# Performance work log

Hardware: AMD Instinct MI355X
Metric: run time of the kernel (lower is better)

Reference implementation:

```python
import jax, jax.numpy as jnp
import numpy as np

SD = 4            # sqrt of capsule dim (matrix pose)
STRIDE = 2
LN_EPS = 1e-5


def _unfold(x, k, s):
    # x: [B, N, H, W, A] -> patches [B, N, k, k, Ho, Wo, A]  (matches torch unfold+permute)
    B, N, H, W, A = x.shape
    Ho = (H - k) // s + 1
    Wo = (W - k) // s + 1
    ih = np.arange(Ho)[:, None] * s + np.arange(k)   # [Ho, k]
    iw = np.arange(Wo)[:, None] * s + np.arange(k)   # [Wo, k]
    p = x[:, :, ih]               # [B, N, Ho, k, W, A]
    p = p[:, :, :, :, iw]         # [B, N, Ho, k, Wo, k, A]
    return p.transpose(0, 1, 3, 5, 2, 4, 6)


def _layer_norm(v, g, b):
    mu = jnp.mean(v, axis=-1, keepdims=True)
    var = jnp.mean(jnp.square(v - mu), axis=-1, keepdims=True)
    return (v - mu) * jax.lax.rsqrt(var + LN_EPS) * g + b


def setup_inputs() -> dict:
    key = jax.random.key(0)
    k0, k1, k2 = jax.random.split(key, 3)
    B, N, H, W, A = 64, 32, 16, 16, 16     # batch, in caps, spatial, pose dim
    K, M, D = 3, 32, 16                     # kernel, out caps (conv), out pose dim
    Ho = Wo = (H - K) // STRIDE + 1         # 7
    Nfc, Cls = M * Ho * Wo, 10              # 1568 fc input caps, 10 classes
    x = jax.random.normal(k0, (B, N, H, W, A), dtype=jnp.float32)
    c_conv = np.sqrt(M / (SD * N * K * K)).astype(np.float32)
    w_conv = c_conv * jax.random.normal(k1, (K, K, N, SD, SD, M), dtype=jnp.float32)
    c_fc = np.sqrt(Cls / (SD * Nfc)).astype(np.float32)
    w_fc = c_fc * jax.random.normal(k2, (Nfc, SD, SD, Cls), dtype=jnp.float32)
    return {
        "x": x, "w_conv": w_conv, "w_fc": w_fc,
        "ln1_g": jnp.ones((D,), jnp.float32), "ln1_b": jnp.zeros((D,), jnp.float32),
        "ln2_g": jnp.ones((D,), jnp.float32), "ln2_b": jnp.zeros((D,), jnp.float32),
        "num_routing": 3,
    }


def reference(x, w_conv, w_fc, ln1_g, ln1_b, ln2_g, ln2_b, num_routing):
    B = x.shape[0]
    K, _, N, _, _, M = w_conv.shape
    D = SD * SD
    scale = 1.0 / np.sqrt(D)

    # ---------------- CapsuleCONV (matrix pose) ----------------
    patches = _unfold(x, K, STRIDE)                       # [B,N,K,K,Ho,Wo,A]
    Ho, Wo = patches.shape[4], patches.shape[5]
    inp = patches.reshape(B, N, K, K, Ho, Wo, SD, SD)     # bnklhwax

    # pass 0: uniform routing prior (softmax of zeros) == 1/M
    v = jnp.einsum('bnklhwax,klnxdm->bmhwad', inp, w_conv) / M
    v = _layer_norm(v.reshape(B, M, Ho, Wo, D), ln1_g, ln1_b)
    for _ in range(num_routing - 1):
        v4 = v.reshape(B, M, Ho, Wo, SD, SD)
        logits = jnp.einsum('bnklhwax,klnxdm,bmhwad->bnklmhw', inp, w_conv, v4) * scale
        qk = jax.nn.softmax(logits, axis=4)
        qk = qk / (jnp.sum(qk, axis=4, keepdims=True) + 1e-10)
        v = jnp.einsum('bnklmhw,bnklhwax,klnxdm->bmhwad', qk, inp, w_conv)
        v = _layer_norm(v.reshape(B, M, Ho, Wo, D), ln1_g, ln1_b)

    # ---------------- CapsuleFC (matrix pose) ----------------
    # [B,M,Ho,Wo,D] -> permute(0,4,1,2,3) -> flatten -> [B, M*Ho*Wo, D]
    fc_in = v.transpose(0, 4, 1, 2, 3).reshape(B, D, M * Ho * Wo).transpose(0, 2, 1)
    Nfc, Cls = w_fc.shape[0], w_fc.shape[3]
    _in = fc_in.reshape(B, Nfc, SD, SD)                   # bnax

    u = jnp.einsum('bnax,nxdm->bmad', _in, w_fc) / Cls
    u = _layer_norm(u.reshape(B, Cls, D), ln2_g, ln2_b)
    for _ in range(num_routing - 1):
        u4 = u.reshape(B, Cls, SD, SD)
        logits = jnp.einsum('bnax,nxdm,bmad->bnm', _in, w_fc, u4) * scale
        qk = jax.nn.softmax(logits, axis=2)
        qk = qk / (jnp.sum(qk, axis=2, keepdims=True) + 1e-10)
        u = jnp.einsum('bnm,bnax,nxdm->bmad', qk, _in, w_fc)
        u = _layer_norm(u.reshape(B, Cls, D), ln2_g, ln2_b)

    return u  # [B, num_classes, out_d_capsules]
```

## Files before the change

### kernel.cpp

```cpp
#include <hip/hip_runtime.h>
#include <hip/hip_bf16.h>


#define LN_EPS 1e-5f

typedef _Float16 h2 __attribute__((ext_vector_type(2)));

__device__ __forceinline__ unsigned packh2(float a, float b) {
    const unsigned short ua = __builtin_bit_cast(unsigned short, (_Float16)a);
    const unsigned short ub = __builtin_bit_cast(unsigned short, (_Float16)b);
    return (unsigned)ua | ((unsigned)ub << 16);
}

__device__ __forceinline__ float fdot2u(unsigned a, unsigned b, float c) {
    float d;
    asm("v_dot2_f32_f16 %0, %1, %2, %3" : "=v"(d) : "v"(a), "v"(b), "v"(c));
    return d;
}

template <int CTRL>
__device__ __forceinline__ float dpp_add(float x) {
    return x + __builtin_bit_cast(float,
        __builtin_amdgcn_mov_dpp(__builtin_bit_cast(int, x), CTRL, 0xF, 0xF, false));
}
__device__ __forceinline__ float row16_sum(float x) {
    x = dpp_add<0xB1>(x);
    x = dpp_add<0x4E>(x);
    x = dpp_add<0x124>(x);
    x = dpp_add<0x128>(x);
    return x;
}
__device__ __forceinline__ float swz_xor16(float x) {
    return __builtin_bit_cast(float,
        __builtin_amdgcn_ds_swizzle(__builtin_bit_cast(int, x), 0x401F));
}

__global__ __launch_bounds__(256) void transpose_wconv(
    const float* __restrict__ wconv, unsigned short* __restrict__ wTh)
{
    const int i = blockIdx.x * 256 + threadIdx.x;
    if (i < 147456) {
        const int x = i & 3, d = (i >> 2) & 3, mm = (i >> 4) & 31, r = i >> 9;
        const int n = r / 9, kl = r % 9;
        const float v = wconv[((kl * 32 + n) * 16 + x * 4 + d) * 32 + mm];
        wTh[i] = __builtin_bit_cast(unsigned short, (_Float16)v);
    }
}
__global__ __launch_bounds__(256) void transpose_wfc(
    const float* __restrict__ wfc, float* __restrict__ wT2b)
{
    const int j = blockIdx.x * 256 + threadIdx.x;
    if (j < 401408) {
        const int xd = j & 15, mm = (j >> 4) & 15, n = j >> 8;
        const int x = xd >> 2, dd = xd & 3;
        wT2b[j] = (mm < 10) ? wfc[((n * 4 + x) * 4 + dd) * 10 + mm] : 0.f;
    }
}
__global__ __launch_bounds__(256) void transpose_weights(
    const float* __restrict__ wconv, const float* __restrict__ wfc,
    unsigned short* __restrict__ wTh, float* __restrict__ wT2b)
{
    const int blk = blockIdx.x;
    if (blk < 576) {
        const int i = blk * 256 + threadIdx.x;
        if (i < 147456) {
            const int x = i & 3, d = (i >> 2) & 3, mm = (i >> 4) & 31, r = i >> 9;
            const int n = r / 9, kl = r % 9;
            const float v = wconv[((kl * 32 + n) * 16 + x * 4 + d) * 32 + mm];
            wTh[i] = __builtin_bit_cast(unsigned short, (_Float16)v);
        }
    } else {
        const int j = (blk - 576) * 256 + threadIdx.x;
        if (j < 401408) {
            const int xd = j & 15, mm = (j >> 4) & 15, n = j >> 8;
            const int x = xd >> 2, dd = xd & 3;
            wT2b[j] = (mm < 10) ? wfc[((n * 4 + x) * 4 + dd) * 10 + mm] : 0.f;
        }
    }
}

__global__ __launch_bounds__(256, 5) void conv_routing_kernel(
    const float* __restrict__ x,
    const unsigned short* __restrict__ wTh,
    const float* __restrict__ ln1g,
    const float* __restrict__ ln1b,
    const int*   __restrict__ nroute,
    float* __restrict__ vout)
{
    __shared__ unsigned short s_inp[288][16];
    __shared__ float s_v[32][17];
    __shared__ float s_red[2][32][17];

    const int tid = threadIdx.x;
    const int m   = tid & 31;
    const int g   = (tid >> 5) & 7;
    const int lw  = tid >> 6;
    const int site = blockIdx.x;
    const int b = site / 49, hw = site % 49;
    const int h = hw / 7, w = hw % 7;

    for (int i = tid; i < 1152; i += 256) {
        const int row = i >> 2, q = i & 3;
        const int n = row / 9, kl = row % 9;
        const int k = kl / 3, l = kl % 3;
        const float4 val = *(const float4*)(
            x + ((((b * 32 + n) * 16 + (2 * h + k)) * 16 + (2 * w + l)) * 16 + q * 4));
        uint2 p;
        p.x = packh2(val.x, val.y);
        p.y = packh2(val.z, val.w);
        *(uint2*)(&s_inp[row][q * 4]) = p;
    }
    __syncthreads();

    const int R = *nroute;
    const int nkl0 = g * 36;
    const unsigned short* const wp0 = wTh + (nkl0 * 32 + m) * 16;

    for (int pass = 0; pass < R; ++pass) {
        float vn[16];
#pragma unroll
        for (int i = 0; i < 16; ++i) vn[i] = 0.f;

        if (pass == 0) {
            const unsigned short* wp = wp0;
            for (int t = 0; t < 36; ++t, wp += 512) {
                const uint4 wa = *(const uint4*)(wp);
                const uint4 wb = *(const uint4*)(wp + 8);
                const unsigned wu[8] = { wa.x, wa.y, wa.z, wa.w, wb.x, wb.y, wb.z, wb.w };
                const uint4* rp = (const uint4*)(&s_inp[nkl0 + t][0]);
                const uint4 ua = rp[0], ub = rp[1];
                const unsigned iu[8] = { ua.x, ua.y, ua.z, ua.w, ub.x, ub.y, ub.z, ub.w };
#pragma unroll
                for (int a = 0; a < 4; ++a) {
#pragma unroll
                    for (int d = 0; d < 4; ++d) {
                        vn[a * 4 + d] = fdot2u(iu[a * 2], wu[d * 2],
                            fdot2u(iu[a * 2 + 1], wu[d * 2 + 1], vn[a * 4 + d]));
                    }
                }
            }
        } else {
            float vrr[16];
#pragma unroll
            for (int i = 0; i < 16; ++i) vrr[i] = s_v[m][i];

            const unsigned short* wp = wp0;
            for (int j = 0; j < 18; ++j, wp += 1024) {
                const uint4 wa0 = *(const uint4*)(wp);
                const uint4 wb0 = *(const uint4*)(wp + 8);
                const uint4 wa1 = *(const uint4*)(wp + 512);
                const uint4 wb1 = *(const uint4*)(wp + 520);
                const unsigned wu0[8] = { wa0.x, wa0.y, wa0.z, wa0.w, wb0.x, wb0.y, wb0.z, wb0.w };
                const unsigned wu1[8] = { wa1.x, wa1.y, wa1.z, wa1.w, wb1.x, wb1.y, wb1.z, wb1.w };
                const uint4* rp0 = (const uint4*)(&s_inp[nkl0 + 2 * j][0]);
                const uint4* rp1 = (const uint4*)(&s_inp[nkl0 + 2 * j + 1][0]);
                const uint4 ua0 = rp0[0], ub0 = rp0[1];
                const uint4 ua1 = rp1[0], ub1 = rp1[1];
                const unsigned iu0[8] = { ua0.x, ua0.y, ua0.z, ua0.w, ub0.x, ub0.y, ub0.z, ub0.w };
                const unsigned iu1[8] = { ua1.x, ua1.y, ua1.z, ua1.w, ub1.x, ub1.y, ub1.z, ub1.w };

                float uh0[16], uh1[16];
#pragma unroll
                for (int a = 0; a < 4; ++a) {
#pragma unroll
                    for (int d = 0; d < 4; ++d) {
                        uh0[a * 4 + d] = fdot2u(iu0[a * 2], wu0[d * 2],
                            fdot2u(iu0[a * 2 + 1], wu0[d * 2 + 1], 0.f));
                        uh1[a * 4 + d] = fdot2u(iu1[a * 2], wu1[d * 2],
                            fdot2u(iu1[a * 2 + 1], wu1[d * 2 + 1], 0.f));
                    }
                }

                float p0 = 0.f, p1 = 0.f, q0 = 0.f, q1 = 0.f;
#pragma unroll
                for (int i = 0; i < 16; i += 2) {
                    const float c0 = vrr[i], c1 = vrr[i + 1];
                    p0 = fmaf(uh0[i], c0, p0);
                    q0 = fmaf(uh0[i + 1], c1, q0);
                    p1 = fmaf(uh1[i], c0, p1);
                    q1 = fmaf(uh1[i + 1], c1, q1);
                }
                const float e0 = __expf((p0 + q0) * 0.25f);
                const float e1 = __expf((p1 + q1) * 0.25f);

                float sm0 = row16_sum(e0);
                float sm1 = row16_sum(e1);
                sm0 += swz_xor16(sm0);
                sm1 += swz_xor16(sm1);

                const float qk0 = e0 * __builtin_amdgcn_rcpf(sm0 * (1.f + 1e-10f));
                const float qk1 = e1 * __builtin_amdgcn_rcpf(sm1 * (1.f + 1e-10f));
#pragma unroll
                for (int i = 0; i < 16; ++i) {
                    vn[i] = fmaf(qk0, uh0[i], vn[i]);
                    vn[i] = fmaf(qk1, uh1[i], vn[i]);
                }
            }
        }

#pragma unroll
        for (int i = 0; i < 16; ++i) vn[i] += __shfl_xor(vn[i], 32, 64);

        if (lw >= 2) {
#pragma unroll
            for (int i = 0; i < 16; ++i) s_red[lw - 2][m][i] = vn[i];
        }
        __syncthreads();
        if (lw < 2) {
#pragma unroll
            for (int i = 0; i < 16; ++i) vn[i] += s_red[lw][m][i];
            if (lw == 1) {
#pragma unroll
                for (int i = 0; i < 16; ++i) s_red[1][m][i] = vn[i];
            }
        }
        __syncthreads();
        if (lw == 0) {
#pragma unroll
            for (int i = 0; i < 16; ++i) vn[i] += s_red[1][m][i];
            const float scale = pass ? 1.f : (1.f / 32.f);
            float mu = 0.f;
#pragma unroll
            for (int i = 0; i < 16; ++i) { vn[i] *= scale; mu += vn[i]; }
            mu *= (1.f / 16.f);
            float var = 0.f;
#pragma unroll
            for (int i = 0; i < 16; ++i) {
                const float d0 = vn[i] - mu;
                var = fmaf(d0, d0, var);
            }
            var *= (1.f / 16.f);
            const float inv = rsqrtf(var + LN_EPS);
#pragma unroll
            for (int i = 0; i < 16; ++i)
                s_v[m][i] = (vn[i] - mu) * inv * ln1g[i] + ln1b[i];
        }
        __syncthreads();
    }

    for (int p = tid; p < 512; p += 256) {
        const int mm = p >> 4, i = p & 15;
        vout[((b * 32 + mm) * 49 + hw) * 16 + i] = s_v[mm][i];
    }
}

__global__ __launch_bounds__(512, 4) void fc_pass(
    const float* __restrict__ fcin,
    const float* __restrict__ wT2b,
    const float* __restrict__ prev,
    const float* __restrict__ ln2g,
    const float* __restrict__ ln2b,
    const int*   __restrict__ nroute,
    const int    pass,
    float* __restrict__ pout)
{
    __shared__ float s_red[8][16][17];
    __shared__ float s_u[16][17];

    const int R = *nroute;
    if (pass >= R) return;
    const int blk = blockIdx.x;
    const int b = blk >> 3, c = blk & 7;
    const int tid = threadIdx.x;
    const int ml = tid & 15, grp = tid >> 4;
    const int wv = tid >> 6;

    float ur[16];
    if (pass) {
        if (tid < 256) {
            const int mlf = tid >> 4, ii = tid & 15;
            float s = 0.f;
#pragma unroll
            for (int c2 = 0; c2 < 8; ++c2)
                s += prev[((b * 8 + c2) * 16 + mlf) * 16 + ii];
            if (pass == 1) s *= 0.1f;
            float mu = s;
#pragma unroll
            for (int off = 8; off >= 1; off >>= 1) mu += __shfl_xor(mu, off, 16);
            mu *= (1.f / 16.f);
            const float d0 = s - mu;
            float var = d0 * d0;
#pragma unroll
            for (int off = 8; off >= 1; off >>= 1) var += __shfl_xor(var, off, 16);
            var *= (1.f / 16.f);
            s_u[mlf][ii] = (s - mu) * rsqrtf(var + LN_EPS) * ln2g[ii] + ln2b[ii];
        }
        __syncthreads();
#pragma unroll
        for (int i = 0; i < 16; ++i) ur[i] = s_u[ml][i];
    }

    const float* fb = fcin + (b * 1568 + c * 196) * 16;
    const float* wb = wT2b + (c * 196 * 16) * 16;

    float un[16];
#pragma unroll
    for (int i = 0; i < 16; ++i) un[i] = 0.f;

    for (int t = 0; t < 7; ++t) {
        const int off = t * 32 + grp;
        if (off >= 196) break;
        float iv[16], wv_[16];
        const float* ip = fb + off * 16;
        const float* wp = wb + (off * 16 + ml) * 16;
#pragma unroll
        for (int q = 0; q < 4; ++q) {
            *(float4*)(&iv[q * 4]) = *(const float4*)(ip + q * 4);
            *(float4*)(&wv_[q * 4]) = *(const float4*)(wp + q * 4);
        }
        float vote[16];
#pragma unroll
        for (int a = 0; a < 4; ++a) {
#pragma unroll
            for (int d = 0; d < 4; ++d) {
                float acc = iv[a * 4 + 0] * wv_[0 + d];
                acc = fmaf(iv[a * 4 + 1], wv_[4 + d], acc);
                acc = fmaf(iv[a * 4 + 2], wv_[8 + d], acc);
                acc = fmaf(iv[a * 4 + 3], wv_[12 + d], acc);
                vote[a * 4 + d] = acc;
            }
        }
        if (pass == 0) {
#pragma unroll
            for (int i = 0; i < 16; ++i) un[i] += vote[i];
        } else {
            float l0 = vote[0] * ur[0], l1 = vote[1] * ur[1];
            float l2 = vote[2] * ur[2], l3 = vote[3] * ur[3];
#pragma unroll
            for (int i = 4; i < 16; i += 4) {
                l0 = fmaf(vote[i + 0], ur[i + 0], l0);
                l1 = fmaf(vote[i + 1], ur[i + 1], l1);
                l2 = fmaf(vote[i + 2], ur[i + 2], l2);
                l3 = fmaf(vote[i + 3], ur[i + 3], l3);
            }
            const float lg = ((l0 + l1) + (l2 + l3)) * 0.25f;
            float e = __expf(lg);
            if (ml >= 10) e = 0.f;
            const float sm = row16_sum(e);
            const float qk = e * __builtin_amdgcn_rcpf(sm * (1.f + 1e-10f));
#pragma unroll
            for (int i = 0; i < 16; ++i) un[i] = fmaf(qk, vote[i], un[i]);
        }
    }

#pragma unroll
    for (int i = 0; i < 16; ++i) {
        un[i] += __shfl_xor(un[i], 16, 64);
        un[i] += __shfl_xor(un[i], 32, 64);
    }
    if ((tid & 63) < 16) {
#pragma unroll
        for (int i = 0; i < 16; ++i) s_red[wv][ml][i] = un[i];
    }
    __syncthreads();
    if (tid < 256) {
        const int mlf = tid >> 4, i = tid & 15;
        float s = 0.f;
#pragma unroll
        for (int w2 = 0; w2 < 8; ++w2) s += s_red[w2][mlf][i];
        pout[(blk * 16 + mlf) * 16 + i] = s;
    }
}

__global__ __launch_bounds__(256) void fc_final(
    const float* __restrict__ pA,
    const float* __restrict__ pB,
    const float* __restrict__ ln2g,
    const float* __restrict__ ln2b,
    const int*   __restrict__ nroute,
    float* __restrict__ out)
{
    const int R = *nroute;
    const float* P = ((R - 1) & 1) ? pB : pA;
    const int b = blockIdx.x;
    const int tid = threadIdx.x;
    const int i = tid & 15, ml = tid >> 4;

    float s = 0.f;
#pragma unroll
    for (int c = 0; c < 8; ++c)
        s += P[((b * 8 + c) * 16 + ml) * 16 + i];
    if (R == 1) s *= 0.1f;

    float mu = s;
#pragma unroll
    for (int off = 8; off >= 1; off >>= 1) mu += __shfl_xor(mu, off, 16);
    mu *= (1.f / 16.f);
    const float d0 = s - mu;
    float var = d0 * d0;
#pragma unroll
    for (int off = 8; off >= 1; off >>= 1) var += __shfl_xor(var, off, 16);
    var *= (1.f / 16.f);
    const float r = (s - mu) * rsqrtf(var + LN_EPS) * ln2g[i] + ln2b[i];

    if (ml < 10) out[(b * 10 + ml) * 16 + i] = r;
}

__global__ __launch_bounds__(256, 4) void fc_partial(
    const float* __restrict__ fcin, const float* __restrict__ wT2b,
    const float* __restrict__ u, const int* __restrict__ nroute,
    const int pass, float* __restrict__ partial)
{
    __shared__ float s_red[4][16][17];
    const int R = *nroute;
    if (pass >= R) return;
    const int blk = blockIdx.x;
    const int b = blk >> 3, c = blk & 7;
    const int tid = threadIdx.x;
    const int ml = tid & 15, grp = tid >> 4;
    const int wv = tid >> 6;
    const float* fb = fcin + (b * 1568 + c * 196) * 16;
    const float* wb = wT2b + (c * 196 * 16) * 16;

    float un[16];
#pragma unroll
    for (int i = 0; i < 16; ++i) un[i] = 0.f;
    float ur[16];
    if (pass) {
#pragma unroll
        for (int q = 0; q < 4; ++q)
            *(float4*)(&ur[q * 4]) = *(const float4*)(u + (b * 16 + ml) * 16 + q * 4);
    }
    for (int t = 0; t < 13; ++t) {
        const int off = t * 16 + grp;
        if (off >= 196) break;
        float iv[16], wv_[16];
        const float* ip = fb + off * 16;
        const float* wp = wb + (off * 16 + ml) * 16;
#pragma unroll
        for (int q = 0; q < 4; ++q) {
            *(float4*)(&iv[q * 4]) = *(const float4*)(ip + q * 4);
            *(float4*)(&wv_[q * 4]) = *(const float4*)(wp + q * 4);
        }
        float vote[16];
#pragma unroll
        for (int a = 0; a < 4; ++a) {
#pragma unroll
            for (int d = 0; d < 4; ++d) {
                float acc = iv[a * 4 + 0] * wv_[0 + d];
                acc = fmaf(iv[a * 4 + 1], wv_[4 + d], acc);
                acc = fmaf(iv[a * 4 + 2], wv_[8 + d], acc);
                acc = fmaf(iv[a * 4 + 3], wv_[12 + d], acc);
                vote[a * 4 + d] = acc;
            }
        }
        if (pass == 0) {
#pragma unroll
            for (int i = 0; i < 16; ++i) un[i] += vote[i];
        } else {
            float l0 = vote[0] * ur[0], l1 = vote[1] * ur[1];
            float l2 = vote[2] * ur[2], l3 = vote[3] * ur[3];
#pragma unroll
            for (int i = 4; i < 16; i += 4) {
                l0 = fmaf(vote[i + 0], ur[i + 0], l0);
                l1 = fmaf(vote[i + 1], ur[i + 1], l1);
                l2 = fmaf(vote[i + 2], ur[i + 2], l2);
                l3 = fmaf(vote[i + 3], ur[i + 3], l3);
            }
            const float lg = ((l0 + l1) + (l2 + l3)) * 0.25f;
            float e = __expf(lg);
            if (ml >= 10) e = 0.f;
            float sm = e;
#pragma unroll
            for (int off2 = 8; off2 >= 1; off2 >>= 1)
                sm += __shfl_xor(sm, off2, 16);
            const float qk = e * __builtin_amdgcn_rcpf(sm * (1.f + 1e-10f));
#pragma unroll
            for (int i = 0; i < 16; ++i) un[i] = fmaf(qk, vote[i], un[i]);
        }
    }
#pragma unroll
    for (int i = 0; i < 16; ++i) {
        un[i] += __shfl_xor(un[i], 16, 64);
        un[i] += __shfl_xor(un[i], 32, 64);
    }
    if ((tid & 63) < 16) {
#pragma unroll
        for (int i = 0; i < 16; ++i) s_red[wv][ml][i] = un[i];
    }
    __syncthreads();
    {
        const int mlf = tid >> 4, i = tid & 15;
        const float s = s_red[0][mlf][i] + s_red[1][mlf][i]
                      + s_red[2][mlf][i] + s_red[3][mlf][i];
        partial[(blk * 16 + mlf) * 16 + i] = s;
    }
}

__global__ __launch_bounds__(256) void fc_combine(
    const float* __restrict__ partial, const float* __restrict__ ln2g,
    const float* __restrict__ ln2b, const int* __restrict__ nroute,
    const int pass, float* __restrict__ u, float* __restrict__ out)
{
    const int R = *nroute;
    if (pass >= R) return;
    const int b = blockIdx.x;
    const int tid = threadIdx.x;
    const int i = tid & 15, ml = tid >> 4;
    float s = 0.f;
#pragma unroll
    for (int c = 0; c < 8; ++c)
        s += partial[((b * 8 + c) * 16 + ml) * 16 + i];
    if (pass == 0) s *= 0.1f;
    float mu = s;
#pragma unroll
    for (int off = 8; off >= 1; off >>= 1) mu += __shfl_xor(mu, off, 16);
    mu *= (1.f / 16.f);
    const float d0 = s - mu;
    float var = d0 * d0;
#pragma unroll
    for (int off = 8; off >= 1; off >>= 1) var += __shfl_xor(var, off, 16);
    var *= (1.f / 16.f);
    const float r = (s - mu) * rsqrtf(var + LN_EPS) * ln2g[i] + ln2b[i];
    u[(b * 16 + ml) * 16 + i] = r;
    if (pass == R - 1 && ml < 10) out[(b * 10 + ml) * 16 + i] = r;
}

extern "C" void kernel_launch(void* const* d_in, const int* in_sizes, int n_in,
                              void* d_out, int out_size, void* d_ws, size_t ws_size,
                              hipStream_t stream) {
    const float* x     = (const float*)d_in[0];
    const float* wconv = (const float*)d_in[1];
    const float* wfc   = (const float*)d_in[2];
    const float* ln1g  = (const float*)d_in[3];
    const float* ln1b  = (const float*)d_in[4];
    const float* ln2g  = (const float*)d_in[5];
    const float* ln2b  = (const float*)d_in[6];
    const int*   nrt   = (const int*)d_in[7];
    float* out = (float*)d_out;

    float* vout = (float*)d_ws;

    if (ws_size >= 9076736) {
        float* wT2b = (float*)((char*)d_ws + 6422528);
        float* pA   = (float*)((char*)d_ws + 8028160);
        float* pB   = (float*)((char*)d_ws + 8552448);
        unsigned short* wTh = (unsigned short*)pA;

        hipLaunchKernelGGL(transpose_weights, dim3(2144), dim3(256), 0, stream,
                           wconv, wfc, wTh, wT2b);
        hipLaunchKernelGGL(conv_routing_kernel, dim3(3136), dim3(256), 0, stream,
                           x, wTh, ln1g, ln1b, nrt, vout);
        hipLaunchKernelGGL(fc_pass, dim3(512), dim3(512), 0, stream,
                           vout, wT2b, (const float*)nullptr, ln2g, ln2b, nrt, 0, pA);
        hipLaunchKernelGGL(fc_pass, dim3(512), dim3(512), 0, stream,
                           vout, wT2b, (const float*)pA, ln2g, ln2b, nrt, 1, pB);
        hipLaunchKernelGGL(fc_pass, dim3(512), dim3(512), 0, stream,
                           vout, wT2b, (const float*)pB, ln2g, ln2b, nrt, 2, pA);
        hipLaunchKernelGGL(fc_final, dim3(64), dim3(256), 0, stream,
                           pA, pB, ln2g, ln2b, nrt, out);
    } else {
        unsigned short* wTh = (unsigned short*)((char*)d_ws + 6422528);
        float* wT2b    = (float*)((char*)d_ws + 6422528);
        float* ubuf    = (float*)((char*)d_ws + 8028160);
        float* partial = (float*)((char*)d_ws + 8093696);

        hipLaunchKernelGGL(transpose_wconv, dim3(576), dim3(256), 0, stream,
                           wconv, wTh);
        hipLaunchKernelGGL(conv_routing_kernel, dim3(3136), dim3(256), 0, stream,
                           x, wTh, ln1g, ln1b, nrt, vout);
        hipLaunchKernelGGL(transpose_wfc, dim3(1568), dim3(256), 0, stream,
                           wfc, wT2b);
        for (int pass = 0; pass < 3; ++pass) {
            hipLaunchKernelGGL(fc_partial, dim3(512), dim3(256), 0, stream,
                               vout, wT2b, ubuf, nrt, pass, partial);
            hipLaunchKernelGGL(fc_combine, dim3(64), dim3(256), 0, stream,
                               partial, ln2g, ln2b, nrt, pass, ubuf, out);
        }
    }
}
```

Measured before the change: 293.5 us.

## Process two output sites per conv routing block to reuse weight loads

Measured after the change: 318.8 us. 8.6% more time.

```diff
diff --git a/kernel.cpp b/kernel.cpp
--- a/kernel.cpp
+++ b/kernel.cpp
@@ -79,7 +79,7 @@
     }
 }
 
-__global__ __launch_bounds__(256, 5) void conv_routing_kernel(
+__global__ __launch_bounds__(256, 4) void conv_routing_kernel(
     const float* __restrict__ x,
     const unsigned short* __restrict__ wTh,
     const float* __restrict__ ln1g,
@@ -87,28 +87,31 @@
     const int*   __restrict__ nroute,
     float* __restrict__ vout)
 {
-    __shared__ unsigned short s_inp[288][16];
-    __shared__ float s_v[32][17];
-    __shared__ float s_red[2][32][17];
+    __shared__ unsigned short s_inp[2][288][16];
+    __shared__ float s_v[2][32][17];
+    __shared__ float s_red[2][2][32][17];
 
     const int tid = threadIdx.x;
     const int m   = tid & 31;
     const int g   = (tid >> 5) & 7;
     const int lw  = tid >> 6;
-    const int site = blockIdx.x;
-    const int b = site / 49, hw = site % 49;
-    const int h = hw / 7, w = hw % 7;
-
-    for (int i = tid; i < 1152; i += 256) {
-        const int row = i >> 2, q = i & 3;
+    const int site0 = blockIdx.x * 2;
+
+    for (int i = tid; i < 2304; i += 256) {
+        const int s = (i >= 1152) ? 1 : 0;
+        const int r2 = i - s * 1152;
+        const int row = r2 >> 2, q = r2 & 3;
         const int n = row / 9, kl = row % 9;
         const int k = kl / 3, l = kl % 3;
+        const int site = site0 + s;
+        const int b = site / 49, hw = site % 49;
+        const int h = hw / 7, w = hw % 7;
         const float4 val = *(const float4*)(
             x + ((((b * 32 + n) * 16 + (2 * h + k)) * 16 + (2 * w + l)) * 16 + q * 4));
         uint2 p;
         p.x = packh2(val.x, val.y);
         p.y = packh2(val.z, val.w);
-        *(uint2*)(&s_inp[row][q * 4]) = p;
+        *(uint2*)(&s_inp[s][row][q * 4]) = p;
     }
     __syncthreads();
 
@@ -117,9 +120,9 @@
     const unsigned short* const wp0 = wTh + (nkl0 * 32 + m) * 16;
 
     for (int pass = 0; pass < R; ++pass) {
-        float vn[16];
-#pragma unroll
-        for (int i = 0; i < 16; ++i) vn[i] = 0.f;
+        float vn0[16], vn1[16];
+#pragma unroll
+        for (int i = 0; i < 16; ++i) { vn0[i] = 0.f; vn1[i] = 0.f; }
 
         if (pass == 0) {
             const unsigned short* wp = wp0;
@@ -127,23 +130,36 @@
                 const uint4 wa = *(const uint4*)(wp);
                 const uint4 wb = *(const uint4*)(wp + 8);
                 const unsigned wu[8] = { wa.x, wa.y, wa.z, wa.w, wb.x, wb.y, wb.z, wb.w };
-                const uint4* rp = (const uint4*)(&s_inp[nkl0 + t][0]);
-                const uint4 ua = rp[0], ub = rp[1];
-                const unsigned iu[8] = { ua.x, ua.y, ua.z, ua.w, ub.x, ub.y, ub.z, ub.w };
-#pragma unroll
-                for (int a = 0; a < 4; ++a) {
-#pragma unroll
-                    for (int d = 0; d < 4; ++d) {
-                        vn[a * 4 + d] = fdot2u(iu[a * 2], wu[d * 2],
-                            fdot2u(iu[a * 2 + 1], wu[d * 2 + 1], vn[a * 4 + d]));
+                {
+                    const uint4* rp = (const uint4*)(&s_inp[0][nkl0 + t][0]);
+                    const uint4 ua = rp[0], ub = rp[1];
+                    const unsigned iu[8] = { ua.x, ua.y, ua.z, ua.w, ub.x, ub.y, ub.z, ub.w };
+#pragma unroll
+                    for (int a = 0; a < 4; ++a) {
+#pragma unroll
+                        for (int d = 0; d < 4; ++d) {
+                            vn0[a * 4 + d] = fdot2u(iu[a * 2], wu[d * 2],
+                                fdot2u(iu[a * 2 + 1], wu[d * 2 + 1], vn0[a * 4 + d]));
+                        }
                     }
                 }
+                {
+                    const uint4* rp = (const uint4*)(&s_inp[1][nkl0 + t][0]);
+                    const uint4 ua = rp[0], ub = rp[1];
+                    const unsigned iu[8] = { ua.x, ua.y, ua.z, ua.w, ub.x, ub.y, ub.z, ub.w };
+#pragma unroll
+                    for (int a = 0; a < 4; ++a) {
+#pragma unroll
+                        for (int d = 0; d < 4; ++d) {
+                            vn1[a * 4 + d] = fdot2u(iu[a * 2], wu[d * 2],
+                                fdot2u(iu[a * 2 + 1], wu[d * 2 + 1], vn1[a * 4 + d]));
+                        }
+                    }
+                }
             }
         } else {
-            float vrr[16];
-#pragma unroll
-            for (int i = 0; i < 16; ++i) vrr[i] = s_v[m][i];
-
+            const float* const vcp0 = &s_v[0][m][0];
+            const float* const vcp1 = &s_v[1][m][0];
             const unsigned short* wp = wp0;
             for (int j = 0; j < 18; ++j, wp += 1024) {
                 const uint4 wa0 = *(const uint4*)(wp);
@@ -152,95 +168,173 @@
                 const uint4 wb1 = *(const uint4*)(wp + 520);
                 const unsigned wu0[8] = { wa0.x, wa0.y, wa0.z, wa0.w, wb0.x, wb0.y, wb0.z, wb0.w };
                 const unsigned wu1[8] = { wa1.x, wa1.y, wa1.z, wa1.w, wb1.x, wb1.y, wb1.z, wb1.w };
-                const uint4* rp0 = (const uint4*)(&s_inp[nkl0 + 2 * j][0]);
-                const uint4* rp1 = (const uint4*)(&s_inp[nkl0 + 2 * j + 1][0]);
-                const uint4 ua0 = rp0[0], ub0 = rp0[1];
-                const uint4 ua1 = rp1[0], ub1 = rp1[1];
-                const unsigned iu0[8] = { ua0.x, ua0.y, ua0.z, ua0.w, ub0.x, ub0.y, ub0.z, ub0.w };
-                const unsigned iu1[8] = { ua1.x, ua1.y, ua1.z, ua1.w, ub1.x, ub1.y, ub1.z, ub1.w };
-
-                float uh0[16], uh1[16];
-#pragma unroll
-                for (int a = 0; a < 4; ++a) {
-#pragma unroll
-                    for (int d = 0; d < 4; ++d) {
-                        uh0[a * 4 + d] = fdot2u(iu0[a * 2], wu0[d * 2],
-                            fdot2u(iu0[a * 2 + 1], wu0[d * 2 + 1], 0.f));
-                        uh1[a * 4 + d] = fdot2u(iu1[a * 2], wu1[d * 2],
-                            fdot2u(iu1[a * 2 + 1], wu1[d * 2 + 1], 0.f));
+
+                {
+                    const uint4* rp0 = (const uint4*)(&s_inp[0][nkl0 + 2 * j][0]);
+                    const uint4* rp1 = (const uint4*)(&s_inp[0][nkl0 + 2 * j + 1][0]);
+                    const uint4 ua0 = rp0[0], ub0 = rp0[1];
+                    const uint4 ua1 = rp1[0], ub1 = rp1[1];
+                    const unsigned iu0[8] = { ua0.x, ua0.y, ua0.z, ua0.w, ub0.x, ub0.y, ub0.z, ub0.w };
+                    const unsigned iu1[8] = { ua1.x, ua1.y, ua1.z, ua1.w, ub1.x, ub1.y, ub1.z, ub1.w };
+
+                    float uh0[16], uh1[16];
+#pragma unroll
+                    for (int a = 0; a < 4; ++a) {
+#pragma unroll
+                        for (int d = 0; d < 4; ++d) {
+                            uh0[a * 4 + d] = fdot2u(iu0[a * 2], wu0[d * 2],
+                                fdot2u(iu0[a * 2 + 1], wu0[d * 2 + 1], 0.f));
+                            uh1[a * 4 + d] = fdot2u(iu1[a * 2], wu1[d * 2],
+                                fdot2u(iu1[a * 2 + 1], wu1[d * 2 + 1], 0.f));
+                        }
+                    }
+                    float p0 = 0.f, p1 = 0.f, q0 = 0.f, q1 = 0.f;
+#pragma unroll
+                    for (int i = 0; i < 16; i += 2) {
+                        const float c0 = vcp0[i], c1 = vcp0[i + 1];
+                        p0 = fmaf(uh0[i], c0, p0);
+                        q0 = fmaf(uh0[i + 1], c1, q0);
+                        p1 = fmaf(uh1[i], c0, p1);
+                        q1 = fmaf(uh1[i + 1], c1, q1);
+                    }
+                    const float e0 = __expf((p0 + q0) * 0.25f);
+                    const float e1 = __expf((p1 + q1) * 0.25f);
+                    float sm0 = row16_sum(e0);
+                    float sm1 = row16_sum(e1);
+                    sm0 += swz_xor16(sm0);
+                    sm1 += swz_xor16(sm1);
+                    const float qk0 = e0 * __builtin_amdgcn_rcpf(sm0 * (1.f + 1e-10f));
+                    const float qk1 = e1 * __builtin_amdgcn_rcpf(sm1 * (1.f + 1e-10f));
+#pragma unroll
+                    for (int i = 0; i < 16; ++i) {
+                        vn0[i] = fmaf(qk0, uh0[i], vn0[i]);
+                        vn0[i] = fmaf(qk1, uh1[i], vn0[i]);
                     }
                 }
-
-                float p0 = 0.f, p1 = 0.f, q0 = 0.f, q1 = 0.f;
-#pragma unroll
-                for (int i = 0; i < 16; i += 2) {
-                    const float c0 = vrr[i], c1 = vrr[i + 1];
-                    p0 = fmaf(uh0[i], c0, p0);
-                    q0 = fmaf(uh0[i + 1], c1, q0);
-                    p1 = fmaf(uh1[i], c0, p1);
-                    q1 = fmaf(uh1[i + 1], c1, q1);
+                {
+                    const uint4* rp0 = (const uint4*)(&s_inp[1][nkl0 + 2 * j][0]);
+                    const uint4* rp1 = (const uint4*)(&s_inp[1][nkl0 + 2 * j + 1][0]);
+                    const uint4 ua0 = rp0[0], ub0 = rp0[1];
+                    const uint4 ua1 = rp1[0], ub1 = rp1[1];
+                    const unsigned iu0[8] = { ua0.x, ua0.y, ua0.z, ua0.w, ub0.x, ub0.y, ub0.z, ub0.w };
+                    const unsigned iu1[8] = { ua1.x, ua1.y, ua1.z, ua1.w, ub1.x, ub1.y, ub1.z, ub1.w };
+
+                    float uh0[16], uh1[16];
+#pragma unroll
+                    for (int a = 0; a < 4; ++a) {
+#pragma unroll
+                        for (int d = 0; d < 4; ++d) {
+                            uh0[a * 4 + d] = fdot2u(iu0[a * 2], wu0[d * 2],
+                                fdot2u(iu0[a * 2 + 1], wu0[d * 2 + 1], 0.f));
+                            uh1[a * 4 + d] = fdot2u(iu1[a * 2], wu1[d * 2],
+                                fdot2u(iu1[a * 2 + 1], wu1[d * 2 + 1], 0.f));
+                        }
+                    }
+                    float p0 = 0.f, p1 = 0.f, q0 = 0.f, q1 = 0.f;
+#pragma unroll
+                    for (int i = 0; i < 16; i += 2) {
+                        const float c0 = vcp1[i], c1 = vcp1[i + 1];
+                        p0 = fmaf(uh0[i], c0, p0);
+                        q0 = fmaf(uh0[i + 1], c1, q0);
+                        p1 = fmaf(uh1[i], c0, p1);
+                        q1 = fmaf(uh1[i + 1], c1, q1);
+                    }
+                    const float e0 = __expf((p0 + q0) * 0.25f);
+                    const float e1 = __expf((p1 + q1) * 0.25f);
+                    float sm0 = row16_sum(e0);
+                    float sm1 = row16_sum(e1);
+                    sm0 += swz_xor16(sm0);
+                    sm1 += swz_xor16(sm1);
+                    const float qk0 = e0 * __builtin_amdgcn_rcpf(sm0 * (1.f + 1e-10f));
+                    const float qk1 = e1 * __builtin_amdgcn_rcpf(sm1 * (1.f + 1e-10f));
+#pragma unroll
+                    for (int i = 0; i < 16; ++i) {
+                        vn1[i] = fmaf(qk0, uh0[i], vn1[i]);
+                        vn1[i] = fmaf(qk1, uh1[i], vn1[i]);
+                    }
                 }
-                const float e0 = __expf((p0 + q0) * 0.25f);
-                const float e1 = __expf((p1 + q1) * 0.25f);
-
-                float sm0 = row16_sum(e0);
-                float sm1 = row16_sum(e1);
-                sm0 += swz_xor16(sm0);
-                sm1 += swz_xor16(sm1);
-
-                const float qk0 = e0 * __builtin_amdgcn_rcpf(sm0 * (1.f + 1e-10f));
-                const float qk1 = e1 * __builtin_amdgcn_rcpf(sm1 * (1.f + 1e-10f));
-#pragma unroll
-                for (int i = 0; i < 16; ++i) {
-                    vn[i] = fmaf(qk0, uh0[i], vn[i]);
-                    vn[i] = fmaf(qk1, uh1[i], vn[i]);
-                }
-            }
-        }
-
-#pragma unroll
-        for (int i = 0; i < 16; ++i) vn[i] += __shfl_xor(vn[i], 32, 64);
-
+            }
+        }
+
+#pragma unroll
+        for (int i = 0; i < 16; ++i) {
+            vn0[i] += __shfl_xor(vn0[i], 32, 64);
+            vn1[i] += __shfl_xor(vn1[i], 32, 64);
+        }
         if (lw >= 2) {
 #pragma unroll
-            for (int i = 0; i < 16; ++i) s_red[lw - 2][m][i] = vn[i];
+            for (int i = 0; i < 16; ++i) {
+                s_red[0][lw - 2][m][i] = vn0[i];
+                s_red[1][lw - 2][m][i] = vn1[i];
+            }
         }
         __syncthreads();
         if (lw < 2) {
 #pragma unroll
-            for (int i = 0; i < 16; ++i) vn[i] += s_red[lw][m][i];
+            for (int i = 0; i < 16; ++i) {
+                vn0[i] += s_red[0][lw][m][i];
+                vn1[i] += s_red[1][lw][m][i];
+            }
             if (lw == 1) {
 #pragma unroll
-                for (int i = 0; i < 16; ++i) s_red[1][m][i] = vn[i];
+                for (int i = 0; i < 16; ++i) {
+                    s_red[0][1][m][i] = vn0[i];
+                    s_red[1][1][m][i] = vn1[i];
+                }
             }
         }
         __syncthreads();
         if (lw == 0) {
-#pragma unroll
-            for (int i = 0; i < 16; ++i) vn[i] += s_red[1][m][i];
             const float scale = pass ? 1.f : (1.f / 32.f);
-            float mu = 0.f;
-#pragma unroll
-            for (int i = 0; i < 16; ++i) { vn[i] *= scale; mu += vn[i]; }
-            mu *= (1.f / 16.f);
-            float var = 0.f;
 #pragma unroll
             for (int i = 0; i < 16; ++i) {
-                const float d0 = vn[i] - mu;
-                var = fmaf(d0, d0, var);
-            }
-            var *= (1.f / 16.f);
-            const float inv = rsqrtf(var + LN_EPS);
-#pragma unroll
-            for (int i = 0; i < 16; ++i)
-                s_v[m][i] = (vn[i] - mu) * inv * ln1g[i] + ln1b[i];
+                vn0[i] = (vn0[i] + s_red[0][1][m][i]) * scale;
+                vn1[i] = (vn1[i] + s_red[1][1][m][i]) * scale;
+            }
+            {
+                float mu = 0.f;
+#pragma unroll
+                for (int i = 0; i < 16; ++i) mu += vn0[i];
+                mu *= (1.f / 16.f);
+                float var = 0.f;
+#pragma unroll
+                for (int i = 0; i < 16; ++i) {
+                    const float d0 = vn0[i] - mu;
+                    var = fmaf(d0, d0, var);
+                }
+                var *= (1.f / 16.f);
+                const float inv = rsqrtf(var + LN_EPS);
+#pragma unroll
+                for (int i = 0; i < 16; ++i)
+                    s_v[0][m][i] = (vn0[i] - mu) * inv * ln1g[i] + ln1b[i];
+            }
+            {
+                float mu = 0.f;
+#pragma unroll
+                for (int i = 0; i < 16; ++i) mu += vn1[i];
+                mu *= (1.f / 16.f);
+                float var = 0.f;
+#pragma unroll
+                for (int i = 0; i < 16; ++i) {
+                    const float d0 = vn1[i] - mu;
+                    var = fmaf(d0, d0, var);
+                }
+                var *= (1.f / 16.f);
+                const float inv = rsqrtf(var + LN_EPS);
+#pragma unroll
+                for (int i = 0; i < 16; ++i)
+                    s_v[1][m][i] = (vn1[i] - mu) * inv * ln1g[i] + ln1b[i];
+            }
         }
         __syncthreads();
     }
 
-    for (int p = tid; p < 512; p += 256) {
-        const int mm = p >> 4, i = p & 15;
-        vout[((b * 32 + mm) * 49 + hw) * 16 + i] = s_v[mm][i];
+    for (int p = tid; p < 1024; p += 256) {
+        const int s = p >> 9, r2 = p & 511;
+        const int mm = r2 >> 4, i = r2 & 15;
+        const int site = site0 + s;
+        const int b = site / 49, hw = site % 49;
+        vout[((b * 32 + mm) * 49 + hw) * 16 + i] = s_v[s][mm][i];
     }
 }
 
@@ -539,7 +633,7 @@
 
         hipLaunchKernelGGL(transpose_weights, dim3(2144), dim3(256), 0, stream,
                            wconv, wfc, wTh, wT2b);
-        hipLaunchKernelGGL(conv_routing_kernel, dim3(3136), dim3(256), 0, stream,
+        hipLaunchKernelGGL(conv_routing_kernel, dim3(1568), dim3(256), 0, stream,
                            x, wTh, ln1g, ln1b, nrt, vout);
         hipLaunchKernelGGL(fc_pass, dim3(512), dim3(512), 0, stream,
                            vout, wT2b, (const float*)nullptr, ln2g, ln2b, nrt, 0, pA);
@@ -557,7 +651,7 @@
 
         hipLaunchKernelGGL(transpose_wconv, dim3(576), dim3(256), 0, stream,
                            wconv, wTh);
-        hipLaunchKernelGGL(conv_routing_kernel, dim3(3136), dim3(256), 0, stream,
+        hipLaunchKernelGGL(conv_routing_kernel, dim3(1568), dim3(256), 0, stream,
                            x, wTh, ln1g, ln1b, nrt, vout);
         hipLaunchKernelGGL(transpose_wfc, dim3(1568), dim3(256), 0, stream,
                            wfc, wT2b);
```
